# Kernel optimization log

Hardware: AMD Instinct MI355X
Metric: run time of the kernel (lower is better)

## Reference

```python
import jax, jax.numpy as jnp
import numpy as np

INT_MIN, INT_MAX = -128.0, 127.0   # signed 8-bit weight range
UINT_MAX = 255.0                   # unsigned 8-bit activation range


def weight_quant(W):
    """Int8 per-tensor fixed-point (power-of-two scale from max-abs stats), STE."""
    max_abs = jax.lax.stop_gradient(jnp.max(jnp.abs(W)))
    # restrict threshold to power of two (ceil), scale = 2^e / 2^(bw-1)
    exp = jnp.ceil(jnp.log2(jnp.maximum(max_abs, 1e-12)))
    scale = jnp.exp2(exp) / 128.0
    q = jnp.clip(jnp.round(W / scale), INT_MIN, INT_MAX) * scale
    return W + jax.lax.stop_gradient(q - W)


def act_quant_relu(x, scale):
    """QuantReLU: relu then unsigned 8-bit quant-dequant with per-tensor scale, STE."""
    x = jax.nn.relu(x)
    s = jax.lax.stop_gradient(scale)
    q = jnp.clip(jnp.round(x / s), 0.0, UINT_MAX) * s
    return x + jax.lax.stop_gradient(q - x)


def setup_inputs() -> dict:
    key = jax.random.key(0)
    ks = jax.random.split(key, 9)
    B, D, U = 500000, 256, 64
    x = jax.random.normal(ks[0], (B, D), dtype=jnp.float32)
    W1 = jax.random.normal(ks[1], (U, D), dtype=jnp.float32) * (1.0 / np.sqrt(D))
    b1 = jax.random.normal(ks[2], (U,), dtype=jnp.float32) * 0.01
    W2 = jax.random.normal(ks[3], (U, U), dtype=jnp.float32) * (1.0 / np.sqrt(U))
    b2 = jax.random.normal(ks[4], (U,), dtype=jnp.float32) * 0.01
    Wout = jax.random.normal(ks[5], (1, U), dtype=jnp.float32) * (1.0 / np.sqrt(U))
    bout = jax.random.normal(ks[6], (1,), dtype=jnp.float32) * 0.01
    a1 = jax.random.uniform(ks[7], (), dtype=jnp.float32, minval=0.01, maxval=0.1)
    a2 = jax.random.uniform(ks[8], (), dtype=jnp.float32, minval=0.01, maxval=0.1)
    return {"x": x, "W1": W1, "b1": b1, "W2": W2, "b2": b2,
            "Wout": Wout, "bout": bout, "a1": a1, "a2": a2}


def reference(x, W1, b1, W2, b2, Wout, bout, a1, a2):
    # layer 1: quant-linear -> QuantReLU (dropout is identity at inference)
    h = x @ weight_quant(W1).T + b1
    h = act_quant_relu(h, a1)
    # layer 2
    h = h @ weight_quant(W2).T + b2
    h = act_quant_relu(h, a2)
    # output quant-linear (no activation quant)
    return h @ weight_quant(Wout).T + bout
```

## Files before the change

kernel.cpp:

```cpp
#include <hip/hip_runtime.h>

typedef __attribute__((ext_vector_type(8))) short s16x8;
typedef __attribute__((ext_vector_type(4))) float f32x4;

union FragU {
    unsigned int u[4];
    uint4 v;
    s16x8 s;
};

__device__ __forceinline__ float pow2_scale_inv(float ma, float& scale) {
    ma = fmaxf(ma, 1e-12f);
    unsigned u = __float_as_uint(ma);
    int E = (int)((u >> 23) & 255u);
    int ce = ((u & 0x7fffffu) == 0u) ? (E - 127) : (E - 126);
    int se = ce - 7;
    scale = __uint_as_float((unsigned)(se + 127) << 23);
    return __uint_as_float((unsigned)(127 - se) << 23);
}

__global__ __launch_bounds__(256) void fused_kernel(
    const float* __restrict__ x,
    const float* __restrict__ W1,
    const float* __restrict__ b1,
    const float* __restrict__ W2,
    const float* __restrict__ b2,
    const float* __restrict__ Wo,
    const float* __restrict__ boutp,
    const float* __restrict__ a1p,
    const float* __restrict__ a2p,
    float* __restrict__ out,
    int ntiles, int nwaves) {

    __shared__ __align__(16) unsigned short w1f[16384];
    __shared__ __align__(16) unsigned short w2f[4096];
    __shared__ __align__(16) unsigned short stg[4][1024];
    __shared__ float redm[12];

    const int t = threadIdx.x;
    const int lane = t & 63;
    const int wv = t >> 6;

    float4 w1v[16];
    float4 w2v[4];
    float m1 = 0.f, m2 = 0.f, mo = 0.f;
    #pragma unroll
    for (int k = 0; k < 16; ++k) {
        w1v[k] = *(const float4*)(W1 + 4 * (t + 256 * k));
        m1 = fmaxf(m1, fmaxf(fmaxf(fabsf(w1v[k].x), fabsf(w1v[k].y)),
                             fmaxf(fabsf(w1v[k].z), fabsf(w1v[k].w))));
    }
    #pragma unroll
    for (int k = 0; k < 4; ++k) {
        w2v[k] = *(const float4*)(W2 + 4 * (t + 256 * k));
        m2 = fmaxf(m2, fmaxf(fmaxf(fabsf(w2v[k].x), fabsf(w2v[k].y)),
                             fmaxf(fabsf(w2v[k].z), fabsf(w2v[k].w))));
    }
    if (t < 64) mo = fabsf(Wo[t]);

    #pragma unroll
    for (int m = 1; m < 64; m <<= 1) {
        m1 = fmaxf(m1, __shfl_xor(m1, m, 64));
        m2 = fmaxf(m2, __shfl_xor(m2, m, 64));
        mo = fmaxf(mo, __shfl_xor(mo, m, 64));
    }
    if (lane == 0) { redm[wv] = m1; redm[4 + wv] = m2; redm[8 + wv] = mo; }
    __syncthreads();
    m1 = fmaxf(fmaxf(redm[0], redm[1]), fmaxf(redm[2], redm[3]));
    m2 = fmaxf(fmaxf(redm[4], redm[5]), fmaxf(redm[6], redm[7]));
    mo = fmaxf(fmaxf(redm[8], redm[9]), fmaxf(redm[10], redm[11]));

    float s1, s2, so;
    const float i1 = pow2_scale_inv(m1, s1);
    const float i2 = pow2_scale_inv(m2, s2);
    const float io = pow2_scale_inv(mo, so);

    #pragma unroll
    for (int k = 0; k < 16; ++k) {
        const int i0 = 4 * (t + 256 * k);
        float q4[4] = {w1v[k].x, w1v[k].y, w1v[k].z, w1v[k].w};
        #pragma unroll
        for (int e = 0; e < 4; ++e) {
            const int i = i0 + e;
            float q = fminf(fmaxf(rintf(q4[e] * i1), -128.f), 127.f);
            const int u = i >> 8, kk = i & 255;
            const int c = u >> 4, ccb = u & 15, s = kk >> 5, gg = (kk >> 3) & 3, j = kk & 7;
            w1f[((s * 4 + c) * 64 + gg * 16 + ccb) * 8 + j] =
                (unsigned short)(__float_as_uint(q) >> 16);
        }
    }
    #pragma unroll
    for (int k = 0; k < 4; ++k) {
        const int i0 = 4 * (t + 256 * k);
        float q4[4] = {w2v[k].x, w2v[k].y, w2v[k].z, w2v[k].w};
        #pragma unroll
        for (int e = 0; e < 4; ++e) {
            const int i = i0 + e;
            float q = fminf(fmaxf(rintf(q4[e] * i2), -128.f), 127.f);
            const int v = i >> 6, kk = i & 63;
            const int c = v >> 4, ccb = v & 15, s = kk >> 5, gg = (kk >> 3) & 3, j = kk & 7;
            w2f[((s * 4 + c) * 64 + gg * 16 + ccb) * 8 + j] =
                (unsigned short)(__float_as_uint(q) >> 16);
        }
    }
    __syncthreads();

    const float a1 = a1p[0], a2 = a2p[0];
    const float boutv = boutp[0];
    const float c21 = a1 * s2;
    const float c3  = a2 * so;

    const int cc = lane & 15;
    const int g  = lane >> 4;

    float b1c[4], b2c[4], wqc[4];
    #pragma unroll
    for (int c = 0; c < 4; ++c) {
        b1c[c] = b1[c * 16 + cc];
        b2c[c] = b2[c * 16 + cc];
        wqc[c] = fminf(fmaxf(rintf(Wo[c * 16 + cc] * io), -128.f), 127.f);
    }

    unsigned short* st = stg[wv];
    const int gw0 = blockIdx.x * 4 + wv;

    float4 xv[16];
    if (gw0 < ntiles) {
        const float* xp = x + (size_t)(gw0 * 16 + cc) * 256 + g * 8;
        #pragma unroll
        for (int ks = 0; ks < 8; ++ks) {
            xv[2 * ks]     = *(const float4*)(xp + ks * 32);
            xv[2 * ks + 1] = *(const float4*)(xp + ks * 32 + 4);
        }
    }

    for (int tile = gw0; tile < ntiles; tile += nwaves) {
        const int nt = tile + nwaves;
        const bool pf = nt < ntiles;
        const float* xpn = x + (size_t)(nt * 16 + cc) * 256 + g * 8;

        f32x4 acc[4];
        #pragma unroll
        for (int c = 0; c < 4; ++c) acc[c] = (f32x4){0.f, 0.f, 0.f, 0.f};

        #pragma unroll
        for (int ks = 0; ks < 8; ++ks) {
            float xf[8] = {xv[2*ks].x, xv[2*ks].y, xv[2*ks].z, xv[2*ks].w,
                           xv[2*ks+1].x, xv[2*ks+1].y, xv[2*ks+1].z, xv[2*ks+1].w};
            FragU hi, lo, lo2;
            #pragma unroll
            for (int p = 0; p < 4; ++p) {
                float f0 = xf[2*p], f1 = xf[2*p+1];
                unsigned u0 = __float_as_uint(f0), u1 = __float_as_uint(f1);
                unsigned h0 = u0 & 0xffff0000u, h1 = u1 & 0xffff0000u;
                hi.u[p] = (u0 >> 16) | h1;
                float r0 = f0 - __uint_as_float(h0);
                float r1 = f1 - __uint_as_float(h1);
                unsigned v0 = __float_as_uint(r0), v1 = __float_as_uint(r1);
                unsigned m0 = v0 & 0xffff0000u, m1_ = v1 & 0xffff0000u;
                lo.u[p] = (v0 >> 16) | m1_;
                float q0 = r0 - __uint_as_float(m0);
                float q1 = r1 - __uint_as_float(m1_);
                lo2.u[p] = (__float_as_uint(q0) >> 16) | (__float_as_uint(q1) & 0xffff0000u);
            }
            if (pf) {
                xv[2 * ks]     = *(const float4*)(xpn + ks * 32);
                xv[2 * ks + 1] = *(const float4*)(xpn + ks * 32 + 4);
            }
            #pragma unroll
            for (int c = 0; c < 4; ++c) {
                FragU b;
                b.v = *(const uint4*)&w1f[((ks * 4 + c) * 64 + lane) * 8];
                acc[c] = __builtin_amdgcn_mfma_f32_16x16x32_bf16(hi.s,  b.s, acc[c], 0, 0, 0);
                acc[c] = __builtin_amdgcn_mfma_f32_16x16x32_bf16(lo.s,  b.s, acc[c], 0, 0, 0);
                acc[c] = __builtin_amdgcn_mfma_f32_16x16x32_bf16(lo2.s, b.s, acc[c], 0, 0, 0);
            }
        }

        #pragma unroll
        for (int c = 0; c < 4; ++c) {
            #pragma unroll
            for (int j = 0; j < 4; ++j) {
                float h = fmaf(acc[c][j], s1, b1c[c]);
                h = fmaxf(h, 0.f);
                float n = rintf(h / a1);
                n = fminf(n, 255.f);
                const int r = g * 4 + j;
                const int u = c * 16 + cc;
                const int pos = ((u >> 5) * 64 + ((u >> 3) & 3) * 16 + r) * 8 + (u & 7);
                st[pos] = (unsigned short)(__float_as_uint(n) >> 16);
            }
        }
        asm volatile("s_waitcnt lgkmcnt(0)" ::: "memory");

        s16x8 afrag[2];
        #pragma unroll
        for (int s = 0; s < 2; ++s) {
            FragU a;
            a.v = *(const uint4*)&st[(s * 64 + lane) * 8];
            afrag[s] = a.s;
        }

        f32x4 acc2[4];
        #pragma unroll
        for (int c = 0; c < 4; ++c) acc2[c] = (f32x4){0.f, 0.f, 0.f, 0.f};
        #pragma unroll
        for (int s = 0; s < 2; ++s) {
            #pragma unroll
            for (int c = 0; c < 4; ++c) {
                FragU b;
                b.v = *(const uint4*)&w2f[((s * 4 + c) * 64 + lane) * 8];
                acc2[c] = __builtin_amdgcn_mfma_f32_16x16x32_bf16(afrag[s], b.s, acc2[c], 0, 0, 0);
            }
        }

        float psum[4] = {0.f, 0.f, 0.f, 0.f};
        #pragma unroll
        for (int c = 0; c < 4; ++c) {
            #pragma unroll
            for (int j = 0; j < 4; ++j) {
                float h = fmaf(acc2[c][j], c21, b2c[c]);
                h = fmaxf(h, 0.f);
                float n = rintf(h / a2);
                n = fminf(n, 255.f);
                psum[j] = fmaf(n, wqc[c], psum[j]);
            }
        }
        #pragma unroll
        for (int j = 0; j < 4; ++j) {
            #pragma unroll
            for (int mask = 1; mask < 16; mask <<= 1)
                psum[j] += __shfl_xor(psum[j], mask, 16);
        }

        if (cc == 0) {
            float4 o;
            o.x = fmaf(psum[0], c3, boutv);
            o.y = fmaf(psum[1], c3, boutv);
            o.z = fmaf(psum[2], c3, boutv);
            o.w = fmaf(psum[3], c3, boutv);
            *(float4*)(out + (size_t)tile * 16 + g * 4) = o;
        }
    }
}

extern "C" void kernel_launch(void* const* d_in, const int* in_sizes, int n_in,
                              void* d_out, int out_size, void* d_ws, size_t ws_size,
                              hipStream_t stream) {
    const float* x    = (const float*)d_in[0];
    const float* W1   = (const float*)d_in[1];
    const float* b1   = (const float*)d_in[2];
    const float* W2   = (const float*)d_in[3];
    const float* b2   = (const float*)d_in[4];
    const float* Wout = (const float*)d_in[5];
    const float* bout = (const float*)d_in[6];
    const float* a1   = (const float*)d_in[7];
    const float* a2   = (const float*)d_in[8];
    float* out = (float*)d_out;

    const int rows = in_sizes[0] / 256;
    const int ntiles = rows / 16;

    int blocks = 768;
    if (blocks * 4 > ntiles) blocks = (ntiles + 3) / 4;
    const int nwaves = blocks * 4;

    fused_kernel<<<blocks, 256, 0, stream>>>(x, W1, b1, W2, b2, Wout, bout,
                                             a1, a2, out, ntiles, nwaves);
}
```

Before: 116.7 us.

## Halve x prefetch registers, raise occupancy, replace divides with split reciprocal

Reduces register pressure so three blocks can be resident per CU. The x prefetch buffer shrinks from a full 256-float row to a rolling half-row ring, and the preloaded weight arrays are dropped in favour of reloading W1/W2 from global memory. Per-element divisions by a1/a2 become a multiply by a double-derived hi/lo reciprocal pair, and the bf16 packing uses v_perm. Occupancy and latency hiding should improve, but the extra weight reload costs a little, and reciprocal rounding could differ from true division at rounding ties.

```diff
diff --git a/kernel.cpp b/kernel.cpp
--- a/kernel.cpp
+++ b/kernel.cpp
@@ -19,7 +19,11 @@
     return __uint_as_float((unsigned)(127 - se) << 23);
 }
 
-__global__ __launch_bounds__(256) void fused_kernel(
+__device__ __forceinline__ unsigned pack_hi16(unsigned u0, unsigned u1) {
+    return __builtin_amdgcn_perm(u1, u0, 0x07060302u);
+}
+
+__global__ __launch_bounds__(256, 3) void fused_kernel(
     const float* __restrict__ x,
     const float* __restrict__ W1,
     const float* __restrict__ b1,
@@ -41,20 +45,18 @@
     const int lane = t & 63;
     const int wv = t >> 6;
 
-    float4 w1v[16];
-    float4 w2v[4];
     float m1 = 0.f, m2 = 0.f, mo = 0.f;
-    #pragma unroll
+    #pragma unroll 4
     for (int k = 0; k < 16; ++k) {
-        w1v[k] = *(const float4*)(W1 + 4 * (t + 256 * k));
-        m1 = fmaxf(m1, fmaxf(fmaxf(fabsf(w1v[k].x), fabsf(w1v[k].y)),
-                             fmaxf(fabsf(w1v[k].z), fabsf(w1v[k].w))));
+        float4 v = *(const float4*)(W1 + 4 * (t + 256 * k));
+        m1 = fmaxf(m1, fmaxf(fmaxf(fabsf(v.x), fabsf(v.y)),
+                             fmaxf(fabsf(v.z), fabsf(v.w))));
     }
     #pragma unroll
     for (int k = 0; k < 4; ++k) {
-        w2v[k] = *(const float4*)(W2 + 4 * (t + 256 * k));
-        m2 = fmaxf(m2, fmaxf(fmaxf(fabsf(w2v[k].x), fabsf(w2v[k].y)),
-                             fmaxf(fabsf(w2v[k].z), fabsf(w2v[k].w))));
+        float4 v = *(const float4*)(W2 + 4 * (t + 256 * k));
+        m2 = fmaxf(m2, fmaxf(fmaxf(fabsf(v.x), fabsf(v.y)),
+                             fmaxf(fabsf(v.z), fabsf(v.w))));
     }
     if (t < 64) mo = fabsf(Wo[t]);
 
@@ -75,10 +77,17 @@
     const float i2 = pow2_scale_inv(m2, s2);
     const float io = pow2_scale_inv(mo, so);
 
-    #pragma unroll
+    const float a1 = a1p[0], a2 = a2p[0];
+    const double d1 = 1.0 / (double)a1;
+    const float i1h = (float)d1, i1l = (float)(d1 - (double)i1h);
+    const double d2 = 1.0 / (double)a2;
+    const float i2h = (float)d2, i2l = (float)(d2 - (double)i2h);
+
+    #pragma unroll 4
     for (int k = 0; k < 16; ++k) {
         const int i0 = 4 * (t + 256 * k);
-        float q4[4] = {w1v[k].x, w1v[k].y, w1v[k].z, w1v[k].w};
+        float4 v = *(const float4*)(W1 + i0);
+        float q4[4] = {v.x, v.y, v.z, v.w};
         #pragma unroll
         for (int e = 0; e < 4; ++e) {
             const int i = i0 + e;
@@ -92,20 +101,20 @@
     #pragma unroll
     for (int k = 0; k < 4; ++k) {
         const int i0 = 4 * (t + 256 * k);
-        float q4[4] = {w2v[k].x, w2v[k].y, w2v[k].z, w2v[k].w};
+        float4 v = *(const float4*)(W2 + i0);
+        float q4[4] = {v.x, v.y, v.z, v.w};
         #pragma unroll
         for (int e = 0; e < 4; ++e) {
             const int i = i0 + e;
             float q = fminf(fmaxf(rintf(q4[e] * i2), -128.f), 127.f);
-            const int v = i >> 6, kk = i & 63;
-            const int c = v >> 4, ccb = v & 15, s = kk >> 5, gg = (kk >> 3) & 3, j = kk & 7;
+            const int vv = i >> 6, kk = i & 63;
+            const int c = vv >> 4, ccb = vv & 15, s = kk >> 5, gg = (kk >> 3) & 3, j = kk & 7;
             w2f[((s * 4 + c) * 64 + gg * 16 + ccb) * 8 + j] =
                 (unsigned short)(__float_as_uint(q) >> 16);
         }
     }
     __syncthreads();
 
-    const float a1 = a1p[0], a2 = a2p[0];
     const float boutv = boutp[0];
     const float c21 = a1 * s2;
     const float c3  = a2 * so;
@@ -124,20 +133,21 @@
     unsigned short* st = stg[wv];
     const int gw0 = blockIdx.x * 4 + wv;
 
-    float4 xv[16];
+    float4 xv[8];
     if (gw0 < ntiles) {
-        const float* xp = x + (size_t)(gw0 * 16 + cc) * 256 + g * 8;
-        #pragma unroll
-        for (int ks = 0; ks < 8; ++ks) {
-            xv[2 * ks]     = *(const float4*)(xp + ks * 32);
-            xv[2 * ks + 1] = *(const float4*)(xp + ks * 32 + 4);
+        const float* xp0 = x + (size_t)(gw0 * 16 + cc) * 256 + g * 8;
+        #pragma unroll
+        for (int s = 0; s < 4; ++s) {
+            xv[2 * s]     = *(const float4*)(xp0 + s * 32);
+            xv[2 * s + 1] = *(const float4*)(xp0 + s * 32 + 4);
         }
     }
 
     for (int tile = gw0; tile < ntiles; tile += nwaves) {
+        const float* xp = x + (size_t)(tile * 16 + cc) * 256 + g * 8;
         const int nt = tile + nwaves;
         const bool pf = nt < ntiles;
-        const float* xpn = x + (size_t)(nt * 16 + cc) * 256 + g * 8;
+        const float* xpn = pf ? (x + (size_t)(nt * 16 + cc) * 256 + g * 8) : xp;
 
         f32x4 acc[4];
         #pragma unroll
@@ -145,27 +155,28 @@
 
         #pragma unroll
         for (int ks = 0; ks < 8; ++ks) {
-            float xf[8] = {xv[2*ks].x, xv[2*ks].y, xv[2*ks].z, xv[2*ks].w,
-                           xv[2*ks+1].x, xv[2*ks+1].y, xv[2*ks+1].z, xv[2*ks+1].w};
+            const int sl = ks & 3;
+            const float4 A = xv[2 * sl];
+            const float4 B = xv[2 * sl + 1];
+
+            const float* pb = (ks < 4) ? (xp + (ks + 4) * 32) : (xpn + (ks - 4) * 32);
+            xv[2 * sl]     = *(const float4*)(pb);
+            xv[2 * sl + 1] = *(const float4*)(pb + 4);
+
+            float f[8] = {A.x, A.y, A.z, A.w, B.x, B.y, B.z, B.w};
             FragU hi, lo, lo2;
             #pragma unroll
             for (int p = 0; p < 4; ++p) {
-                float f0 = xf[2*p], f1 = xf[2*p+1];
-                unsigned u0 = __float_as_uint(f0), u1 = __float_as_uint(f1);
-                unsigned h0 = u0 & 0xffff0000u, h1 = u1 & 0xffff0000u;
-                hi.u[p] = (u0 >> 16) | h1;
-                float r0 = f0 - __uint_as_float(h0);
-                float r1 = f1 - __uint_as_float(h1);
-                unsigned v0 = __float_as_uint(r0), v1 = __float_as_uint(r1);
-                unsigned m0 = v0 & 0xffff0000u, m1_ = v1 & 0xffff0000u;
-                lo.u[p] = (v0 >> 16) | m1_;
-                float q0 = r0 - __uint_as_float(m0);
-                float q1 = r1 - __uint_as_float(m1_);
-                lo2.u[p] = (__float_as_uint(q0) >> 16) | (__float_as_uint(q1) & 0xffff0000u);
-            }
-            if (pf) {
-                xv[2 * ks]     = *(const float4*)(xpn + ks * 32);
-                xv[2 * ks + 1] = *(const float4*)(xpn + ks * 32 + 4);
+                const float f0 = f[2 * p], f1 = f[2 * p + 1];
+                const unsigned u0 = __float_as_uint(f0), u1 = __float_as_uint(f1);
+                hi.u[p] = pack_hi16(u0, u1);
+                const float r0 = f0 - __uint_as_float(u0 & 0xffff0000u);
+                const float r1 = f1 - __uint_as_float(u1 & 0xffff0000u);
+                const unsigned v0 = __float_as_uint(r0), v1 = __float_as_uint(r1);
+                lo.u[p] = pack_hi16(v0, v1);
+                const float q0 = r0 - __uint_as_float(v0 & 0xffff0000u);
+                const float q1 = r1 - __uint_as_float(v1 & 0xffff0000u);
+                lo2.u[p] = pack_hi16(__float_as_uint(q0), __float_as_uint(q1));
             }
             #pragma unroll
             for (int c = 0; c < 4; ++c) {
@@ -183,7 +194,7 @@
             for (int j = 0; j < 4; ++j) {
                 float h = fmaf(acc[c][j], s1, b1c[c]);
                 h = fmaxf(h, 0.f);
-                float n = rintf(h / a1);
+                float n = rintf(fmaf(h, i1l, h * i1h));
                 n = fminf(n, 255.f);
                 const int r = g * 4 + j;
                 const int u = c * 16 + cc;
@@ -221,7 +232,7 @@
             for (int j = 0; j < 4; ++j) {
                 float h = fmaf(acc2[c][j], c21, b2c[c]);
                 h = fmaxf(h, 0.f);
-                float n = rintf(h / a2);
+                float n = rintf(fmaf(h, i2l, h * i2h));
                 n = fminf(n, 255.f);
                 psum[j] = fmaf(n, wqc[c], psum[j]);
             }
```

Result: faster. 106.5 us (-8.7%).
